# Kernel tuning notes

Hardware: AMD Instinct MI355X
Metric: run time of the kernel (lower is better)

The kernel has to match this reference:

```python
import jax, jax.numpy as jnp
import numpy as np

NEG_SLOPE = 0.2
EPS = 1e-5

N_NODES = 50000
N_GRAPHS = 500
NODES_PER_GRAPH = 100
N_EDGES = 500000
F_IN = 16
F_GRAPH = 4
HID = 64
N_CLASSES = 2


def setup_inputs() -> dict:
    key = jax.random.key(0)
    ks = jax.random.split(key, 32)
    x = jax.random.normal(ks[0], (N_NODES, F_IN), dtype=jnp.float32)
    # intra-graph random edges: dst lives in the same 100-node block as src
    src = jax.random.randint(ks[1], (N_EDGES,), 0, N_NODES)
    dst = (src // NODES_PER_GRAPH) * NODES_PER_GRAPH + jax.random.randint(ks[2], (N_EDGES,), 0, NODES_PER_GRAPH)
    edge_index = jnp.stack([src, dst]).astype(jnp.int64)
    graph_input = jax.random.normal(ks[3], (N_GRAPHS, F_GRAPH), dtype=jnp.float32)
    batch = (jnp.arange(N_NODES) // NODES_PER_GRAPH).astype(jnp.int64)

    def w(k, shape, scale=0.1):
        return (jax.random.normal(k, shape, dtype=jnp.float32) * scale)

    inp = dict(x=x, edge_index=edge_index, graph_input=graph_input, batch=batch)
    # GraphNorm params
    inp['gn_w'] = jnp.ones((F_IN,), jnp.float32)
    inp['gn_b'] = w(ks[4], (F_IN,))
    inp['gn_ms'] = jnp.ones((F_IN,), jnp.float32)
    inp['W1'] = w(ks[5], (F_IN, 4 * HID))
    inp['as1'] = w(ks[6], (4, HID)); inp['ad1'] = w(ks[7], (4, HID))
    inp['b1'] = w(ks[8], (4 * HID,))
    inp['W2'] = w(ks[9], (4 * HID, 4 * HID))
    inp['as2'] = w(ks[10], (4, HID)); inp['ad2'] = w(ks[11], (4, HID))
    inp['b2'] = w(ks[12], (4 * HID,))
    inp['W3'] = w(ks[13], (4 * HID, HID))
    inp['as3'] = w(ks[14], (1, HID)); inp['ad3'] = w(ks[15], (1, HID))
    inp['b3'] = w(ks[16], (HID,))
    # BatchNorm1d (eval mode) over [HID + F_GRAPH]
    D = HID + F_GRAPH
    inp['bn_g'] = 1.0 + w(ks[17], (D,))
    inp['bn_b'] = w(ks[18], (D,))
    inp['bn_m'] = jnp.zeros((D,), jnp.float32)
    inp['bn_v'] = jnp.ones((D,), jnp.float32)
    # Dense head
    inp['Wd1'] = w(ks[19], (D, HID)); inp['bd1'] = w(ks[20], (HID,))
    inp['Wd2'] = w(ks[21], (HID, HID)); inp['bd2'] = w(ks[22], (HID,))
    inp['Wo'] = w(ks[23], (HID, N_CLASSES)); inp['bo'] = w(ks[24], (N_CLASSES,))
    return inp


def _segment_softmax(e, seg, n):
    m = jax.ops.segment_max(e, seg, num_segments=n)
    ex = jnp.exp(e - m[seg])
    s = jax.ops.segment_sum(ex, seg, num_segments=n)
    return ex / s[seg]


def _gat_conv(x, src, dst, W, att_src, att_dst, b):
    N = x.shape[0]
    H, C = att_src.shape
    loop = jnp.arange(N)
    src = jnp.concatenate([src, loop])  # PyG GATConv adds self-loops
    dst = jnp.concatenate([dst, loop])
    h = (x @ W).reshape(N, H, C)
    a_src = (h * att_src).sum(-1)  # [N,H]
    a_dst = (h * att_dst).sum(-1)
    e = jax.nn.leaky_relu(a_src[src] + a_dst[dst], NEG_SLOPE)  # [E,H]
    alpha = _segment_softmax(e, dst, N)
    out = jax.ops.segment_sum(h[src] * alpha[:, :, None], dst, num_segments=N)
    return out.reshape(N, H * C) + b


def _graph_norm(x, batch, n_graphs, w, b, ms):
    cnt = jax.ops.segment_sum(jnp.ones((x.shape[0],), x.dtype), batch, num_segments=n_graphs)[:, None]
    mean = jax.ops.segment_sum(x, batch, num_segments=n_graphs) / cnt
    out = x - mean[batch] * ms
    var = jax.ops.segment_sum(out * out, batch, num_segments=n_graphs) / cnt
    return w * out / jnp.sqrt(var[batch] + EPS) + b


def _global_mean_pool(x, batch, n_graphs):
    cnt = jax.ops.segment_sum(jnp.ones((x.shape[0],), x.dtype), batch, num_segments=n_graphs)[:, None]
    return jax.ops.segment_sum(x, batch, num_segments=n_graphs) / cnt


def reference(x, edge_index, graph_input, batch,
              gn_w, gn_b, gn_ms,
              W1, as1, ad1, b1,
              W2, as2, ad2, b2,
              W3, as3, ad3, b3,
              bn_g, bn_b, bn_m, bn_v,
              Wd1, bd1, Wd2, bd2, Wo, bo):
    src, dst = edge_index[0], edge_index[1]
    G = graph_input.shape[0]
    h = _graph_norm(x, batch, G, gn_w, gn_b, gn_ms)
    # dropout is a no-op in eval
    h = jax.nn.elu(_gat_conv(h, src, dst, W1, as1, ad1, b1))
    h = jax.nn.elu(_gat_conv(h, src, dst, W2, as2, ad2, b2))
    h = _gat_conv(h, src, dst, W3, as3, ad3, b3)
    g = _global_mean_pool(h, batch, G)
    g = jnp.concatenate([g, graph_input], axis=1)
    g = (g - bn_m) / jnp.sqrt(bn_v + EPS) * bn_g + bn_b  # BatchNorm1d eval
    g = jax.nn.selu(g @ Wd1 + bd1)
    g = jax.nn.selu(g @ Wd2 + bd2)
    g = g @ Wo + bo
    return jax.nn.softmax(g, axis=1)
```

## Files before the change

kernel.cpp:

```cpp
#include <hip/hip_runtime.h>
#include <math.h>

#define N_NODES 50000
#define N_ROWS_PAD 50048
#define N_GRAPHS 500
#define NPG 100
#define N_EDGES 500000
#define F_IN 16
#define HID 64
#define EW_CAP 1408

#define SELU_SCALE 1.0507009873554804934193349852946f
#define SELU_ALPHA 1.6732632423543772848170429916717f

typedef __attribute__((ext_vector_type(8))) short short8;
typedef __attribute__((ext_vector_type(8))) unsigned short ushort8;
typedef __attribute__((ext_vector_type(4))) float floatx4;

__device__ __forceinline__ float lrelu(float x){ return x > 0.f ? x : 0.2f * x; }
__device__ __forceinline__ float eluf(float x){ return x > 0.f ? x : expf(x) - 1.f; }
__device__ __forceinline__ float seluf(float x){
    return x > 0.f ? SELU_SCALE * x : SELU_SCALE * (SELU_ALPHA * (expf(x) - 1.f));
}
__device__ __forceinline__ unsigned short f2bf(float x){
    unsigned u = __float_as_uint(x);
    return (unsigned short)((u + 0x7FFFu + ((u >> 16) & 1u)) >> 16);
}
__device__ __forceinline__ float bf2f(unsigned short u){
    return __uint_as_float((unsigned)u << 16);
}
__device__ __forceinline__ float bf2f_lo(unsigned u){
    return __uint_as_float(u << 16);
}
__device__ __forceinline__ float bf2f_hi(unsigned u){
    return __uint_as_float(u & 0xFFFF0000u);
}

__global__ void k_count(const int* __restrict__ dst, int* __restrict__ counts){
    int e = blockIdx.x * 256 + threadIdx.x;
    if (e < N_EDGES) atomicAdd(&counts[dst[e]], 1);
}

__global__ void k_local_scan(const int* __restrict__ counts, int* __restrict__ local_off,
                             int* __restrict__ graph_tot){
    __shared__ int s[128];
    int g = blockIdx.x, t = threadIdx.x;
    int v = (t < NPG) ? counts[g * NPG + t] : 0;
    s[t] = v; __syncthreads();
    for (int o = 1; o < 128; o <<= 1){
        int x = (t >= o) ? s[t - o] : 0;
        __syncthreads();
        s[t] += x;
        __syncthreads();
    }
    if (t < NPG) local_off[g * NPG + t] = s[t] - v;
    if (t == 127) graph_tot[g] = s[127];
}

__global__ void k_graph_scan(const int* __restrict__ graph_tot, int* __restrict__ graph_base){
    __shared__ int s[512];
    int t = threadIdx.x;
    int v = (t < N_GRAPHS) ? graph_tot[t] : 0;
    s[t] = v; __syncthreads();
    for (int o = 1; o < 512; o <<= 1){
        int x = (t >= o) ? s[t - o] : 0;
        __syncthreads();
        s[t] += x;
        __syncthreads();
    }
    if (t < N_GRAPHS) graph_base[t] = s[t] - v;
}

__global__ void k_off(const int* __restrict__ local_off, const int* __restrict__ graph_base,
                      int* __restrict__ node_off, int* __restrict__ write_ptr){
    int n = blockIdx.x * 256 + threadIdx.x;
    if (n < N_NODES){
        int v = local_off[n] + graph_base[n / NPG];
        node_off[n] = v;
        write_ptr[n] = v;
    }
}

__global__ void k_scatter(const int* __restrict__ src, const int* __restrict__ dst,
                          int* __restrict__ write_ptr, int* __restrict__ csr){
    int e = blockIdx.x * 256 + threadIdx.x;
    if (e < N_EDGES){
        int d = dst[e];
        int pos = atomicAdd(&write_ptr[d], 1);
        int b = (d / NPG) * NPG;
        csr[pos] = (src[e] - b) | ((d - b) << 8);
    }
}

__global__ void k_gnorm(const float* __restrict__ x, const float* __restrict__ w,
                        const float* __restrict__ b, const float* __restrict__ ms,
                        float* __restrict__ y){
    __shared__ float sx[NPG * F_IN];
    __shared__ float red[16][16];
    __shared__ float meanS[16], varS[16];
    int g = blockIdx.x, t = threadIdx.x;
    for (int idx = t; idx < NPG * F_IN; idx += 256) sx[idx] = x[g * NPG * F_IN + idx];
    __syncthreads();
    int f = t & 15, grp = t >> 4;
    float p = 0.f;
    for (int i = grp; i < NPG; i += 16) p += sx[i * 16 + f];
    red[grp][f] = p; __syncthreads();
    if (t < 16){
        float s = 0.f;
        for (int i = 0; i < 16; i++) s += red[i][t];
        meanS[t] = s * (1.f / 100.f);
    }
    __syncthreads();
    float mm = meanS[f] * ms[f];
    p = 0.f;
    for (int i = grp; i < NPG; i += 16){ float v = sx[i * 16 + f] - mm; p += v * v; }
    red[grp][f] = p; __syncthreads();
    if (t < 16){
        float s = 0.f;
        for (int i = 0; i < 16; i++) s += red[i][t];
        varS[t] = s * (1.f / 100.f);
    }
    __syncthreads();
    for (int idx = t; idx < NPG * F_IN; idx += 256){
        int ff = idx & 15;
        float v = sx[idx] - meanS[ff] * ms[ff];
        y[g * NPG * F_IN + idx] = w[ff] * v * rsqrtf(varS[ff] + 1e-5f) + b[ff];
    }
}

__global__ void __launch_bounds__(256)
k_gemm_tiled(const float* __restrict__ X, const float* __restrict__ W,
             unsigned short* __restrict__ Ybf, int N){
    __shared__ float As[64][17];
    __shared__ float Bs[16][256];
    int t = threadIdx.x;
    int r0 = blockIdx.x * 64;
    {
        int row = t >> 2, kq = t & 3;
        float4 v = (r0 + row < N) ? *(const float4*)&X[(size_t)(r0 + row) * 16 + kq * 4]
                                  : make_float4(0.f, 0.f, 0.f, 0.f);
        As[row][kq * 4 + 0] = v.x; As[row][kq * 4 + 1] = v.y;
        As[row][kq * 4 + 2] = v.z; As[row][kq * 4 + 3] = v.w;
    }
    for (int i = t; i < 1024; i += 256)
        *(float4*)&Bs[0][i * 4] = *(const float4*)&W[i * 4];
    __syncthreads();

    int c4 = t & 15, rsub = t >> 4;
    float acc[4][16];
    #pragma unroll
    for (int i = 0; i < 4; i++)
        #pragma unroll
        for (int j = 0; j < 16; j++) acc[i][j] = 0.f;

    for (int k = 0; k < 16; k++){
        float a_[4];
        #pragma unroll
        for (int i = 0; i < 4; i++) a_[i] = As[rsub + 16 * i][k];
        float4 b0 = *(const float4*)&Bs[k][c4 * 4];
        float4 b1 = *(const float4*)&Bs[k][64 + c4 * 4];
        float4 b2 = *(const float4*)&Bs[k][128 + c4 * 4];
        float4 b3 = *(const float4*)&Bs[k][192 + c4 * 4];
        float bv[16] = {b0.x, b0.y, b0.z, b0.w, b1.x, b1.y, b1.z, b1.w,
                        b2.x, b2.y, b2.z, b2.w, b3.x, b3.y, b3.z, b3.w};
        #pragma unroll
        for (int i = 0; i < 4; i++)
            #pragma unroll
            for (int j = 0; j < 16; j++) acc[i][j] = fmaf(a_[i], bv[j], acc[i][j]);
    }
    #pragma unroll
    for (int i = 0; i < 4; i++){
        int row = r0 + rsub + 16 * i;
        if (row < N){
            ushort8 ua, ub;
            #pragma unroll
            for (int m = 0; m < 8; m++){
                ua[m] = f2bf(acc[i][(m & 3) * 4 + (m >> 2)]);
                ub[m] = f2bf(acc[i][(m & 3) * 4 + 2 + (m >> 2)]);
            }
            *(ushort8*)&Ybf[(size_t)row * 256 + c4 * 16]     = ua;
            *(ushort8*)&Ybf[(size_t)row * 256 + c4 * 16 + 8] = ub;
        }
    }
}

__global__ void k_pack_w(const float* __restrict__ W, unsigned short* __restrict__ Wp,
                         int K, int OUT){
    int idx = blockIdx.x * 256 + threadIdx.x;
    if (idx >= K * OUT) return;
    int k = idx / OUT, n = idx - k * OUT;
    Wp[(((k >> 3) * OUT) + n) * 8 + (k & 7)] = f2bf(W[idx]);
}

template<int COLB>
__global__ void __launch_bounds__(256)
k_gemm_mfma(const unsigned short* __restrict__ Xb,
            const unsigned short* __restrict__ Wp,
            unsigned short* __restrict__ Ybf, int N, int K, int OUT){
    int b = blockIdx.x;
    if (COLB == 4){
        int xcd = b & 7, idx = b >> 3;
        b = xcd * (int)(gridDim.x >> 3) + idx;
    }
    int cb = b & (COLB - 1);
    int rb = b / COLB;

    int t = threadIdx.x;
    int wave = t >> 6, lane = t & 63;
    int quad = lane >> 4, ln = lane & 15;
    int r0 = rb * 64 + wave * 16;
    int c0 = cb * 64;

    floatx4 acc[4];
    #pragma unroll
    for (int f = 0; f < 4; f++) acc[f] = (floatx4){0.f, 0.f, 0.f, 0.f};

    const unsigned short* aptr = Xb + (size_t)(r0 + ln) * K + quad * 8;
    for (int kt = 0; kt < K; kt += 32){
        short8 a = *(const short8*)(aptr + kt);
        int kc = (kt >> 3) + quad;
        #pragma unroll
        for (int f = 0; f < 4; f++){
            short8 bfr = *(const short8*)(Wp + ((size_t)kc * OUT + c0 + f * 16 + ln) * 8);
            acc[f] = __builtin_amdgcn_mfma_f32_16x16x32_bf16(a, bfr, acc[f], 0, 0, 0);
        }
    }
    int rowb = r0 + quad * 4;
    #pragma unroll
    for (int f = 0; f < 4; f++){
        int col = c0 + f * 16 + ln;
        #pragma unroll
        for (int rg = 0; rg < 4; rg++){
            int row = rowb + rg;
            if (row < N) Ybf[(size_t)row * OUT + col] = f2bf(acc[f][rg]);
        }
    }
}

template<int ILVIN>
__global__ void __launch_bounds__(512)
k_fused4(const unsigned short* __restrict__ hbf, const float* __restrict__ as,
         const float* __restrict__ ad, const float* __restrict__ bias,
         const int* __restrict__ csr, const int* __restrict__ noff,
         const int* __restrict__ cnt, unsigned short* __restrict__ out_bf){
    __shared__ __align__(16) unsigned short hl[NPG * 256];
    __shared__ __align__(16) unsigned int edl[EW_CAP][4];
    __shared__ __align__(16) float asrcl[NPG * 4], adstl[NPG * 4];
    __shared__ __align__(16) float wselfl[NPG * 4], rsuml[NPG * 4];
    __shared__ int offl[NPG], cntl[NPG];

    int g = blockIdx.x, t = threadIdx.x;
    int wave = t >> 6, lane = t & 63;
    int base = g * NPG;

    int ebeg = noff[base];
    int etot = noff[base + NPG - 1] + cnt[base + NPG - 1] - ebeg;
    int eln = etot < EW_CAP ? etot : EW_CAP;

    if (ILVIN){
        const ushort8* hsrc = (const ushort8*)(hbf + (size_t)base * 256);
        for (int i = t; i < NPG * 32; i += 512) ((ushort8*)hl)[i] = hsrc[i];
    } else {
        for (int i = t; i < NPG * 16; i += 512){
            int node = i >> 4, c4 = i & 15;
            const unsigned short* hr = hbf + (size_t)(base + node) * 256 + c4 * 4;
            ushort4 f0 = *(const ushort4*)(hr);
            ushort4 f1 = *(const ushort4*)(hr + 64);
            ushort4 f2 = *(const ushort4*)(hr + 128);
            ushort4 f3 = *(const ushort4*)(hr + 192);
            ushort8 lo, hi;
            lo[0] = f0.x; lo[1] = f1.x; lo[2] = f2.x; lo[3] = f3.x;
            lo[4] = f0.y; lo[5] = f1.y; lo[6] = f2.y; lo[7] = f3.y;
            hi[0] = f0.z; hi[1] = f1.z; hi[2] = f2.z; hi[3] = f3.z;
            hi[4] = f0.w; hi[5] = f1.w; hi[6] = f2.w; hi[7] = f3.w;
            *(ushort8*)&hl[node * 256 + c4 * 16]     = lo;
            *(ushort8*)&hl[node * 256 + c4 * 16 + 8] = hi;
        }
    }
    for (int i = t; i < eln; i += 512) edl[i][2] = (unsigned)csr[ebeg + i];
    if (t < NPG){ offl[t] = noff[base + t]; cntl[t] = cnt[base + t]; }
    __syncthreads();

    {
        int cl = lane & 15, nsub = lane >> 4;
        float av[4][4], dv[4][4];
        #pragma unroll
        for (int hh = 0; hh < 4; hh++){
            float4 a4 = *(const float4*)&as[hh * 64 + cl * 4];
            float4 d4 = *(const float4*)&ad[hh * 64 + cl * 4];
            av[hh][0] = a4.x; av[hh][1] = a4.y; av[hh][2] = a4.z; av[hh][3] = a4.w;
            dv[hh][0] = d4.x; dv[hh][1] = d4.y; dv[hh][2] = d4.z; dv[hh][3] = d4.w;
        }
        for (int g0 = wave * 4; g0 < NPG; g0 += 32){
            int n = g0 + nsub;
            ushort8 lo = *(const ushort8*)&hl[n * 256 + cl * 16];
            ushort8 hi = *(const ushort8*)&hl[n * 256 + cl * 16 + 8];
            float ps[4] = {0.f, 0.f, 0.f, 0.f}, pd[4] = {0.f, 0.f, 0.f, 0.f};
            #pragma unroll
            for (int k = 0; k < 2; k++){
                #pragma unroll
                for (int hh = 0; hh < 4; hh++){
                    float x = bf2f(lo[k * 4 + hh]);
                    ps[hh] = fmaf(x, av[hh][k], ps[hh]);
                    pd[hh] = fmaf(x, dv[hh][k], pd[hh]);
                }
            }
            #pragma unroll
            for (int k = 0; k < 2; k++){
                #pragma unroll
                for (int hh = 0; hh < 4; hh++){
                    float x = bf2f(hi[k * 4 + hh]);
                    ps[hh] = fmaf(x, av[hh][k + 2], ps[hh]);
                    pd[hh] = fmaf(x, dv[hh][k + 2], pd[hh]);
                }
            }
            #pragma unroll
            for (int o = 8; o >= 1; o >>= 1){
                #pragma unroll
                for (int hh = 0; hh < 4; hh++){
                    ps[hh] += __shfl_xor(ps[hh], o);
                    pd[hh] += __shfl_xor(pd[hh], o);
                }
            }
            if (cl == 0){
                *(float4*)&asrcl[n * 4] = make_float4(ps[0], ps[1], ps[2], ps[3]);
                *(float4*)&adstl[n * 4] = make_float4(pd[0], pd[1], pd[2], pd[3]);
            }
        }
    }
    __syncthreads();

    for (int i = t; i < eln; i += 512){
        unsigned sd = edl[i][2];
        int s = sd & 0xFF, d = sd >> 8;
        float4 av = *(const float4*)&asrcl[s * 4];
        float4 dv = *(const float4*)&adstl[d * 4];
        unsigned w0 = f2bf(expf(lrelu(av.x + dv.x)));
        unsigned w1 = f2bf(expf(lrelu(av.y + dv.y)));
        unsigned w2 = f2bf(expf(lrelu(av.z + dv.z)));
        unsigned w3 = f2bf(expf(lrelu(av.w + dv.w)));
        edl[i][0] = w0 | (w1 << 16);
        edl[i][1] = w2 | (w3 << 16);
    }
    __syncthreads();

    if (t < NPG){
        int d = t;
        float4 av = *(const float4*)&asrcl[d * 4];
        float4 dv = *(const float4*)&adstl[d * 4];
        float ws0 = expf(lrelu(av.x + dv.x));
        float ws1 = expf(lrelu(av.y + dv.y));
        float ws2 = expf(lrelu(av.z + dv.z));
        float ws3 = expf(lrelu(av.w + dv.w));
        float s0 = ws0, s1 = ws1, s2 = ws2, s3 = ws3;
        int ebg = offl[d] - ebeg, n = cntl[d];
        for (int j = 0; j < n; j++){
            uint2 v = *(const uint2*)&edl[ebg + j][0];
            s0 += bf2f_lo(v.x); s1 += bf2f_hi(v.x);
            s2 += bf2f_lo(v.y); s3 += bf2f_hi(v.y);
        }
        *(float4*)&wselfl[d * 4] = make_float4(ws0, ws1, ws2, ws3);
        *(float4*)&rsuml[d * 4]  = make_float4(1.f / s0, 1.f / s1, 1.f / s2, 1.f / s3);
    }
    __syncthreads();

    float b0 = bias[lane], b1 = bias[64 + lane], b2 = bias[128 + lane], b3 = bias[192 + lane];
    for (int d = wave; d < NPG; d += 8){
        float4 ws = *(const float4*)&wselfl[d * 4];
        float4 rs = *(const float4*)&rsuml[d * 4];
        ushort4 hv = *(const ushort4*)&hl[d * 256 + lane * 4];
        float a0 = ws.x * bf2f(hv.x);
        float a1 = ws.y * bf2f(hv.y);
        float a2 = ws.z * bf2f(hv.z);
        float a3 = ws.w * bf2f(hv.w);
        int ebg = offl[d] - ebeg, n = cntl[d];
        int j = 0;
        #pragma unroll 1
        for (; j + 4 <= n; j += 4){
            #pragma unroll
            for (int k = 0; k < 4; k++){
                uint4 v = *(const uint4*)&edl[ebg + j + k][0];
                int s = (int)(v.z & 0xFFu);
                ushort4 x = *(const ushort4*)&hl[s * 256 + lane * 4];
                a0 = fmaf(bf2f_lo(v.x), bf2f(x.x), a0);
                a1 = fmaf(bf2f_hi(v.x), bf2f(x.y), a1);
                a2 = fmaf(bf2f_lo(v.y), bf2f(x.z), a2);
                a3 = fmaf(bf2f_hi(v.y), bf2f(x.w), a3);
            }
        }
        for (; j < n; j++){
            uint4 v = *(const uint4*)&edl[ebg + j][0];
            int s = (int)(v.z & 0xFFu);
            ushort4 x = *(const ushort4*)&hl[s * 256 + lane * 4];
            a0 = fmaf(bf2f_lo(v.x), bf2f(x.x), a0);
            a1 = fmaf(bf2f_hi(v.x), bf2f(x.y), a1);
            a2 = fmaf(bf2f_lo(v.y), bf2f(x.z), a2);
            a3 = fmaf(bf2f_hi(v.y), bf2f(x.w), a3);
        }
        size_t ob = (size_t)(base + d) * 256 + lane;
        out_bf[ob]       = f2bf(eluf(a0 * rs.x + b0));
        out_bf[ob + 64]  = f2bf(eluf(a1 * rs.y + b1));
        out_bf[ob + 128] = f2bf(eluf(a2 * rs.z + b2));
        out_bf[ob + 192] = f2bf(eluf(a3 * rs.w + b3));
    }
}

__global__ void __launch_bounds__(256)
k_fused1(const unsigned short* __restrict__ hbf, const float* __restrict__ as,
         const float* __restrict__ ad, const float* __restrict__ bias,
         const int* __restrict__ csr, const int* __restrict__ noff,
         const int* __restrict__ cnt, float* __restrict__ out){
    __shared__ __align__(16) unsigned short hl[NPG * 64];
    __shared__ __align__(16) unsigned int edl[EW_CAP][2];
    __shared__ float asrcl[NPG], adstl[NPG];
    __shared__ float wselfl[NPG], rsuml[NPG];
    __shared__ int offl[NPG], cntl[NPG];

    int g = blockIdx.x, t = threadIdx.x;
    int wave = t >> 6, lane = t & 63;
    int base = g * NPG;

    int ebeg = noff[base];
    int etot = noff[base + NPG - 1] + cnt[base + NPG - 1] - ebeg;
    int eln = etot < EW_CAP ? etot : EW_CAP;

    const ushort8* hsrc = (const ushort8*)(hbf + (size_t)base * 64);
    for (int i = t; i < NPG * 8; i += 256) ((ushort8*)hl)[i] = hsrc[i];
    for (int i = t; i < eln; i += 256) edl[i][1] = (unsigned)csr[ebeg + i];
    if (t < NPG){ offl[t] = noff[base + t]; cntl[t] = cnt[base + t]; }
    __syncthreads();

    {
        int cl = lane & 15, nsub = lane >> 4;
        float4 a4 = *(const float4*)&as[cl * 4];
        float4 d4 = *(const float4*)&ad[cl * 4];
        for (int g0 = wave * 4; g0 < NPG; g0 += 16){
            int n = g0 + nsub;
            ushort4 u = *(const ushort4*)&hl[n * 64 + cl * 4];
            float x0 = bf2f(u.x), x1 = bf2f(u.y), x2 = bf2f(u.z), x3 = bf2f(u.w);
            float ps = x0 * a4.x + x1 * a4.y + x2 * a4.z + x3 * a4.w;
            float pd = x0 * d4.x + x1 * d4.y + x2 * d4.z + x3 * d4.w;
            #pragma unroll
            for (int o = 8; o >= 1; o >>= 1){
                ps += __shfl_xor(ps, o);
                pd += __shfl_xor(pd, o);
            }
            if (cl == 0){ asrcl[n] = ps; adstl[n] = pd; }
        }
    }
    __syncthreads();

    for (int i = t; i < eln; i += 256){
        unsigned sd = edl[i][1];
        int s = sd & 0xFF, d = sd >> 8;
        edl[i][0] = (unsigned)f2bf(expf(lrelu(asrcl[s] + adstl[d])));
    }
    __syncthreads();

    if (t < NPG){
        float wsf = expf(lrelu(asrcl[t] + adstl[t]));
        float sum = wsf;
        int ebg = offl[t] - ebeg, n = cntl[t];
        for (int j = 0; j < n; j++) sum += bf2f((unsigned short)edl[ebg + j][0]);
        wselfl[t] = wsf;
        rsuml[t] = 1.f / sum;
    }
    __syncthreads();

    float bl = bias[lane];
    for (int d = wave; d < NPG; d += 4){
        float acc = wselfl[d] * bf2f(hl[d * 64 + lane]);
        int ebg = offl[d] - ebeg, n = cntl[d];
        for (int j = 0; j < n; j++){
            uint2 v = *(const uint2*)&edl[ebg + j][0];
            acc = fmaf(bf2f_lo(v.x), bf2f(hl[(int)(v.y & 0xFFu) * 64 + lane]), acc);
        }
        out[(size_t)(base + d) * 64 + lane] = acc * rsuml[d] + bl;
    }
}

__global__ void k_head(const float* __restrict__ x3, const float* __restrict__ gin,
                       const float* __restrict__ bn_g, const float* __restrict__ bn_b,
                       const float* __restrict__ bn_m, const float* __restrict__ bn_v,
                       const float* __restrict__ Wd1, const float* __restrict__ bd1,
                       const float* __restrict__ Wd2, const float* __restrict__ bd2,
                       const float* __restrict__ Wo, const float* __restrict__ bo,
                       float* __restrict__ out){
    __shared__ float red[256];
    __shared__ float gv[68];
    __shared__ float g2[64];
    __shared__ float g3[64];
    int g = blockIdx.x, t = threadIdx.x;
    int c = t & 63, grp = t >> 6;
    float p = 0.f;
    for (int i = grp; i < NPG; i += 4) p += x3[(g * NPG + i) * 64 + c];
    red[t] = p; __syncthreads();
    if (t < 64){
        float s = red[t] + red[t + 64] + red[t + 128] + red[t + 192];
        float mean = s * (1.f / 100.f);
        gv[t] = (mean - bn_m[t]) * rsqrtf(bn_v[t] + 1e-5f) * bn_g[t] + bn_b[t];
    } else if (t < 68){
        int j = t - 64;
        float v = gin[g * 4 + j];
        gv[t] = (v - bn_m[t]) * rsqrtf(bn_v[t] + 1e-5f) * bn_g[t] + bn_b[t];
    }
    __syncthreads();
    if (t < 64){
        float s = bd1[t];
        for (int i = 0; i < 68; i++) s += gv[i] * Wd1[i * 64 + t];
        g2[t] = seluf(s);
    }
    __syncthreads();
    if (t < 64){
        float s = bd2[t];
        for (int i = 0; i < 64; i++) s += g2[i] * Wd2[i * 64 + t];
        g3[t] = seluf(s);
    }
    __syncthreads();
    if (t == 0){
        float l0 = bo[0], l1 = bo[1];
        for (int i = 0; i < 64; i++){ l0 += g3[i] * Wo[i * 2]; l1 += g3[i] * Wo[i * 2 + 1]; }
        float mx = fmaxf(l0, l1);
        float e0 = expf(l0 - mx), e1 = expf(l1 - mx);
        float inv = 1.f / (e0 + e1);
        out[g * 2] = e0 * inv;
        out[g * 2 + 1] = e1 * inv;
    }
}

extern "C" void kernel_launch(void* const* d_in, const int* in_sizes, int n_in,
                              void* d_out, int out_size, void* d_ws, size_t ws_size,
                              hipStream_t stream){
    const float* x   = (const float*)d_in[0];
    const int*   ei  = (const int*)d_in[1];
    const float* gin = (const float*)d_in[2];
    const float* gn_w = (const float*)d_in[4];
    const float* gn_b = (const float*)d_in[5];
    const float* gn_ms = (const float*)d_in[6];
    const float* W1 = (const float*)d_in[7];
    const float* as1 = (const float*)d_in[8];
    const float* ad1 = (const float*)d_in[9];
    const float* b1 = (const float*)d_in[10];
    const float* W2 = (const float*)d_in[11];
    const float* as2 = (const float*)d_in[12];
    const float* ad2 = (const float*)d_in[13];
    const float* b2 = (const float*)d_in[14];
    const float* W3 = (const float*)d_in[15];
    const float* as3 = (const float*)d_in[16];
    const float* ad3 = (const float*)d_in[17];
    const float* b3 = (const float*)d_in[18];
    const float* bn_g = (const float*)d_in[19];
    const float* bn_b = (const float*)d_in[20];
    const float* bn_m = (const float*)d_in[21];
    const float* bn_v = (const float*)d_in[22];
    const float* Wd1 = (const float*)d_in[23];
    const float* bd1 = (const float*)d_in[24];
    const float* Wd2 = (const float*)d_in[25];
    const float* bd2 = (const float*)d_in[26];
    const float* Wo = (const float*)d_in[27];
    const float* bo = (const float*)d_in[28];
    float* out = (float*)d_out;

    const int* src = ei;
    const int* dst = ei + N_EDGES;

    char* ws = (char*)d_ws;
    size_t off = 0;
    auto alloc = [&](size_t bytes) -> void* {
        void* p = ws + off;
        off = (off + bytes + 255) & ~(size_t)255;
        return p;
    };
    int* counts     = (int*)alloc((size_t)N_NODES * 4);
    int* local_off  = (int*)alloc((size_t)N_NODES * 4);
    int* node_off   = (int*)alloc((size_t)N_NODES * 4);
    int* write_ptr  = (int*)alloc((size_t)N_NODES * 4);
    int* graph_tot  = (int*)alloc(512 * 4);
    int* graph_base = (int*)alloc(512 * 4);
    int* csr        = (int*)alloc((size_t)N_EDGES * 4);
    float* y        = (float*)alloc((size_t)N_NODES * F_IN * 4);
    unsigned short* wp2 = (unsigned short*)alloc((size_t)256 * 256 * 2);
    unsigned short* wp3 = (unsigned short*)alloc((size_t)256 * 64 * 2);
    unsigned short* xbh = (unsigned short*)alloc((size_t)N_NODES * 256 * 2);
    unsigned short* xb  = (unsigned short*)alloc((size_t)N_ROWS_PAD * 256 * 2);
    unsigned short* x3b = (unsigned short*)alloc((size_t)N_NODES * HID * 2);
    float* bufD     = (float*)alloc((size_t)N_NODES * HID * 4);

    hipMemsetAsync(counts, 0, (size_t)N_NODES * 4, stream);
    k_count<<<(N_EDGES + 255) / 256, 256, 0, stream>>>(dst, counts);
    k_local_scan<<<N_GRAPHS, 128, 0, stream>>>(counts, local_off, graph_tot);
    k_graph_scan<<<1, 512, 0, stream>>>(graph_tot, graph_base);
    k_off<<<(N_NODES + 255) / 256, 256, 0, stream>>>(local_off, graph_base, node_off, write_ptr);
    k_scatter<<<(N_EDGES + 255) / 256, 256, 0, stream>>>(src, dst, write_ptr, csr);

    k_pack_w<<<(256 * 256 + 255) / 256, 256, 0, stream>>>(W2, wp2, 256, 256);
    k_pack_w<<<(256 * 64 + 255) / 256, 256, 0, stream>>>(W3, wp3, 256, 64);

    k_gnorm<<<N_GRAPHS, 256, 0, stream>>>(x, gn_w, gn_b, gn_ms, y);

    k_gemm_tiled<<<(N_NODES + 63) / 64, 256, 0, stream>>>(y, W1, xbh, N_NODES);
    k_fused4<1><<<N_GRAPHS, 512, 0, stream>>>(xbh, as1, ad1, b1, csr, node_off, counts, xb);

    k_gemm_mfma<4><<<(N_ROWS_PAD / 64) * 4, 256, 0, stream>>>(xb, wp2, xbh, N_NODES, 256, 256);
    k_fused4<0><<<N_GRAPHS, 512, 0, stream>>>(xbh, as2, ad2, b2, csr, node_off, counts, xb);

    k_gemm_mfma<1><<<N_ROWS_PAD / 64, 256, 0, stream>>>(xb, wp3, x3b, N_NODES, 256, 64);
    k_fused1<<<N_GRAPHS, 256, 0, stream>>>(x3b, as3, ad3, b3, csr, node_off, counts, bufD);

    k_head<<<N_GRAPHS, 256, 0, stream>>>(bufD, gin, bn_g, bn_b, bn_m, bn_v,
                                         Wd1, bd1, Wd2, bd2, Wo, bo, out);
}
```

Baseline: 357.0 us.

## Fold attention vectors into weights and compute GAT logits inside GEMMs

Precomputes W·a_src and W·a_dst products so per-node attention logits come from the input features: layer 1 in the graph-norm kernel, layers 2 and 3 as an extra MFMA tile inside the GEMM. The aggregation kernels no longer compute logits from the bf16 features and load them from small buffers instead. For layer 1 and layer 3 the feature tile is no longer staged in shared memory; gathers read global memory directly, and k_fused1 moves to 512 threads. Logits now come from bf16-rounded folded weights and inputs rather than the bf16 GEMM outputs, which changes rounding. The direct global gathers rely on cache hits instead of LDS.

```diff
diff --git a/kernel.cpp b/kernel.cpp
--- a/kernel.cpp
+++ b/kernel.cpp
@@ -92,9 +92,57 @@
     }
 }
 
+__global__ void k_prep(const float* __restrict__ W1, const float* __restrict__ as1,
+                       const float* __restrict__ ad1,
+                       const float* __restrict__ W2, const float* __restrict__ as2,
+                       const float* __restrict__ ad2,
+                       const float* __restrict__ W3, const float* __restrict__ as3,
+                       const float* __restrict__ ad3,
+                       unsigned short* __restrict__ Wp2, unsigned short* __restrict__ Wp3,
+                       float* __restrict__ M1f,
+                       unsigned short* __restrict__ Mp2, unsigned short* __restrict__ Mp3){
+    int id = blockIdx.x * 256 + threadIdx.x;
+    if (id < 65536){
+        int k = id >> 8, n = id & 255;
+        Wp2[(((k >> 3) * 256) + n) * 8 + (k & 7)] = f2bf(W2[id]);
+    } else if (id < 81920){
+        int i = id - 65536;
+        int k = i >> 6, n = i & 63;
+        Wp3[(((k >> 3) * 64) + n) * 8 + (k & 7)] = f2bf(W3[i]);
+    } else if (id < 82048){
+        int i = id - 81920;
+        int k = i >> 3, j = i & 7;
+        int h = j & 3;
+        const float* a = (j < 4) ? as1 : ad1;
+        float s = 0.f;
+        for (int c = 0; c < 64; c++) s += W1[k * 256 + h * 64 + c] * a[h * 64 + c];
+        M1f[k * 8 + j] = s;
+    } else if (id < 86144){
+        int i = id - 82048;
+        int k = i >> 4, col = i & 15;
+        float s = 0.f;
+        if (col < 8){
+            int h = col & 3;
+            const float* a = (col < 4) ? as2 : ad2;
+            for (int c = 0; c < 64; c++) s += W2[k * 256 + h * 64 + c] * a[h * 64 + c];
+        }
+        Mp2[((k >> 3) * 16 + col) * 8 + (k & 7)] = f2bf(s);
+    } else if (id < 90240){
+        int i = id - 86144;
+        int k = i >> 4, col = i & 15;
+        float s = 0.f;
+        if (col < 2){
+            const float* a = (col == 0) ? as3 : ad3;
+            for (int c = 0; c < 64; c++) s += W3[k * 64 + c] * a[c];
+        }
+        Mp3[((k >> 3) * 16 + col) * 8 + (k & 7)] = f2bf(s);
+    }
+}
+
 __global__ void k_gnorm(const float* __restrict__ x, const float* __restrict__ w,
                         const float* __restrict__ b, const float* __restrict__ ms,
-                        float* __restrict__ y){
+                        const float* __restrict__ M1f,
+                        float* __restrict__ y, float* __restrict__ lg1){
     __shared__ float sx[NPG * F_IN];
     __shared__ float red[16][16];
     __shared__ float meanS[16], varS[16];
@@ -123,8 +171,17 @@
     __syncthreads();
     for (int idx = t; idx < NPG * F_IN; idx += 256){
         int ff = idx & 15;
-        float v = sx[idx] - meanS[ff] * ms[ff];
-        y[g * NPG * F_IN + idx] = w[ff] * v * rsqrtf(varS[ff] + 1e-5f) + b[ff];
+        float v = w[ff] * (sx[idx] - meanS[ff] * ms[ff]) * rsqrtf(varS[ff] + 1e-5f) + b[ff];
+        sx[idx] = v;
+        y[g * NPG * F_IN + idx] = v;
+    }
+    __syncthreads();
+    for (int i = t; i < NPG * 8; i += 256){
+        int n = i >> 3, j = i & 7;
+        float s = 0.f;
+        #pragma unroll
+        for (int ff = 0; ff < 16; ff++) s += sx[n * 16 + ff] * M1f[ff * 8 + j];
+        lg1[(size_t)(g * NPG + n) * 8 + j] = s;
     }
 }
 
@@ -184,19 +241,13 @@
     }
 }
 
-__global__ void k_pack_w(const float* __restrict__ W, unsigned short* __restrict__ Wp,
-                         int K, int OUT){
-    int idx = blockIdx.x * 256 + threadIdx.x;
-    if (idx >= K * OUT) return;
-    int k = idx / OUT, n = idx - k * OUT;
-    Wp[(((k >> 3) * OUT) + n) * 8 + (k & 7)] = f2bf(W[idx]);
-}
-
-template<int COLB>
+template<int COLB, int LG>
 __global__ void __launch_bounds__(256)
 k_gemm_mfma(const unsigned short* __restrict__ Xb,
             const unsigned short* __restrict__ Wp,
-            unsigned short* __restrict__ Ybf, int N, int K, int OUT){
+            const unsigned short* __restrict__ Mp,
+            unsigned short* __restrict__ Ybf, float* __restrict__ lg,
+            int N, int K, int OUT){
     int b = blockIdx.x;
     if (COLB == 4){
         int xcd = b & 7, idx = b >> 3;
@@ -214,6 +265,7 @@
     floatx4 acc[4];
     #pragma unroll
     for (int f = 0; f < 4; f++) acc[f] = (floatx4){0.f, 0.f, 0.f, 0.f};
+    floatx4 accL = (floatx4){0.f, 0.f, 0.f, 0.f};
 
     const unsigned short* aptr = Xb + (size_t)(r0 + ln) * K + quad * 8;
     for (int kt = 0; kt < K; kt += 32){
@@ -224,6 +276,12 @@
             short8 bfr = *(const short8*)(Wp + ((size_t)kc * OUT + c0 + f * 16 + ln) * 8);
             acc[f] = __builtin_amdgcn_mfma_f32_16x16x32_bf16(a, bfr, acc[f], 0, 0, 0);
         }
+        if (LG > 0){
+            if (cb == 0){
+                short8 m = *(const short8*)(Mp + ((size_t)kc * 16 + ln) * 8);
+                accL = __builtin_amdgcn_mfma_f32_16x16x32_bf16(a, m, accL, 0, 0, 0);
+            }
+        }
     }
     int rowb = r0 + quad * 4;
     #pragma unroll
@@ -235,15 +293,24 @@
             if (row < N) Ybf[(size_t)row * OUT + col] = f2bf(acc[f][rg]);
         }
     }
+    if (LG > 0){
+        if (cb == 0 && ln < LG){
+            #pragma unroll
+            for (int rg = 0; rg < 4; rg++){
+                int row = rowb + rg;
+                if (row < N) lg[(size_t)row * LG + ln] = accL[rg];
+            }
+        }
+    }
 }
 
 template<int ILVIN>
 __global__ void __launch_bounds__(512)
-k_fused4(const unsigned short* __restrict__ hbf, const float* __restrict__ as,
-         const float* __restrict__ ad, const float* __restrict__ bias,
+k_fused4(const unsigned short* __restrict__ hbf, const float* __restrict__ lg,
+         const float* __restrict__ bias,
          const int* __restrict__ csr, const int* __restrict__ noff,
          const int* __restrict__ cnt, unsigned short* __restrict__ out_bf){
-    __shared__ __align__(16) unsigned short hl[NPG * 256];
+    __shared__ __align__(16) unsigned short hl[ILVIN ? 16 : NPG * 256];
     __shared__ __align__(16) unsigned int edl[EW_CAP][4];
     __shared__ __align__(16) float asrcl[NPG * 4], adstl[NPG * 4];
     __shared__ __align__(16) float wselfl[NPG * 4], rsuml[NPG * 4];
@@ -257,10 +324,7 @@
     int etot = noff[base + NPG - 1] + cnt[base + NPG - 1] - ebeg;
     int eln = etot < EW_CAP ? etot : EW_CAP;
 
-    if (ILVIN){
-        const ushort8* hsrc = (const ushort8*)(hbf + (size_t)base * 256);
-        for (int i = t; i < NPG * 32; i += 512) ((ushort8*)hl)[i] = hsrc[i];
-    } else {
+    if (!ILVIN){
         for (int i = t; i < NPG * 16; i += 512){
             int node = i >> 4, c4 = i & 15;
             const unsigned short* hr = hbf + (size_t)(base + node) * 256 + c4 * 4;
@@ -278,55 +342,12 @@
         }
     }
     for (int i = t; i < eln; i += 512) edl[i][2] = (unsigned)csr[ebeg + i];
-    if (t < NPG){ offl[t] = noff[base + t]; cntl[t] = cnt[base + t]; }
-    __syncthreads();
-
-    {
-        int cl = lane & 15, nsub = lane >> 4;
-        float av[4][4], dv[4][4];
-        #pragma unroll
-        for (int hh = 0; hh < 4; hh++){
-            float4 a4 = *(const float4*)&as[hh * 64 + cl * 4];
-            float4 d4 = *(const float4*)&ad[hh * 64 + cl * 4];
-            av[hh][0] = a4.x; av[hh][1] = a4.y; av[hh][2] = a4.z; av[hh][3] = a4.w;
-            dv[hh][0] = d4.x; dv[hh][1] = d4.y; dv[hh][2] = d4.z; dv[hh][3] = d4.w;
-        }
-        for (int g0 = wave * 4; g0 < NPG; g0 += 32){
-            int n = g0 + nsub;
-            ushort8 lo = *(const ushort8*)&hl[n * 256 + cl * 16];
-            ushort8 hi = *(const ushort8*)&hl[n * 256 + cl * 16 + 8];
-            float ps[4] = {0.f, 0.f, 0.f, 0.f}, pd[4] = {0.f, 0.f, 0.f, 0.f};
-            #pragma unroll
-            for (int k = 0; k < 2; k++){
-                #pragma unroll
-                for (int hh = 0; hh < 4; hh++){
-                    float x = bf2f(lo[k * 4 + hh]);
-                    ps[hh] = fmaf(x, av[hh][k], ps[hh]);
-                    pd[hh] = fmaf(x, dv[hh][k], pd[hh]);
-                }
-            }
-            #pragma unroll
-            for (int k = 0; k < 2; k++){
-                #pragma unroll
-                for (int hh = 0; hh < 4; hh++){
-                    float x = bf2f(hi[k * 4 + hh]);
-                    ps[hh] = fmaf(x, av[hh][k + 2], ps[hh]);
-                    pd[hh] = fmaf(x, dv[hh][k + 2], pd[hh]);
-                }
-            }
-            #pragma unroll
-            for (int o = 8; o >= 1; o >>= 1){
-                #pragma unroll
-                for (int hh = 0; hh < 4; hh++){
-                    ps[hh] += __shfl_xor(ps[hh], o);
-                    pd[hh] += __shfl_xor(pd[hh], o);
-                }
-            }
-            if (cl == 0){
-                *(float4*)&asrcl[n * 4] = make_float4(ps[0], ps[1], ps[2], ps[3]);
-                *(float4*)&adstl[n * 4] = make_float4(pd[0], pd[1], pd[2], pd[3]);
-            }
-        }
+    if (t < NPG){
+        offl[t] = noff[base + t];
+        cntl[t] = cnt[base + t];
+        const float* lp = lg + (size_t)(base + t) * 8;
+        *(float4*)&asrcl[t * 4] = *(const float4*)lp;
+        *(float4*)&adstl[t * 4] = *(const float4*)(lp + 4);
     }
     __syncthreads();
 
@@ -368,7 +389,8 @@
     for (int d = wave; d < NPG; d += 8){
         float4 ws = *(const float4*)&wselfl[d * 4];
         float4 rs = *(const float4*)&rsuml[d * 4];
-        ushort4 hv = *(const ushort4*)&hl[d * 256 + lane * 4];
+        ushort4 hv = ILVIN ? *(const ushort4*)&hbf[(size_t)(base + d) * 256 + lane * 4]
+                           : *(const ushort4*)&hl[d * 256 + lane * 4];
         float a0 = ws.x * bf2f(hv.x);
         float a1 = ws.y * bf2f(hv.y);
         float a2 = ws.z * bf2f(hv.z);
@@ -381,7 +403,8 @@
             for (int k = 0; k < 4; k++){
                 uint4 v = *(const uint4*)&edl[ebg + j + k][0];
                 int s = (int)(v.z & 0xFFu);
-                ushort4 x = *(const ushort4*)&hl[s * 256 + lane * 4];
+                ushort4 x = ILVIN ? *(const ushort4*)&hbf[(size_t)(base + s) * 256 + lane * 4]
+                                  : *(const ushort4*)&hl[s * 256 + lane * 4];
                 a0 = fmaf(bf2f_lo(v.x), bf2f(x.x), a0);
                 a1 = fmaf(bf2f_hi(v.x), bf2f(x.y), a1);
                 a2 = fmaf(bf2f_lo(v.y), bf2f(x.z), a2);
@@ -391,7 +414,8 @@
         for (; j < n; j++){
             uint4 v = *(const uint4*)&edl[ebg + j][0];
             int s = (int)(v.z & 0xFFu);
-            ushort4 x = *(const ushort4*)&hl[s * 256 + lane * 4];
+            ushort4 x = ILVIN ? *(const ushort4*)&hbf[(size_t)(base + s) * 256 + lane * 4]
+                              : *(const ushort4*)&hl[s * 256 + lane * 4];
             a0 = fmaf(bf2f_lo(v.x), bf2f(x.x), a0);
             a1 = fmaf(bf2f_hi(v.x), bf2f(x.y), a1);
             a2 = fmaf(bf2f_lo(v.y), bf2f(x.z), a2);
@@ -405,12 +429,11 @@
     }
 }
 
-__global__ void __launch_bounds__(256)
-k_fused1(const unsigned short* __restrict__ hbf, const float* __restrict__ as,
-         const float* __restrict__ ad, const float* __restrict__ bias,
+__global__ void __launch_bounds__(512)
+k_fused1(const unsigned short* __restrict__ hbf, const float* __restrict__ lg3,
+         const float* __restrict__ bias,
          const int* __restrict__ csr, const int* __restrict__ noff,
          const int* __restrict__ cnt, float* __restrict__ out){
-    __shared__ __align__(16) unsigned short hl[NPG * 64];
     __shared__ __align__(16) unsigned int edl[EW_CAP][2];
     __shared__ float asrcl[NPG], adstl[NPG];
     __shared__ float wselfl[NPG], rsuml[NPG];
@@ -424,33 +447,16 @@
     int etot = noff[base + NPG - 1] + cnt[base + NPG - 1] - ebeg;
     int eln = etot < EW_CAP ? etot : EW_CAP;
 
-    const ushort8* hsrc = (const ushort8*)(hbf + (size_t)base * 64);
-    for (int i = t; i < NPG * 8; i += 256) ((ushort8*)hl)[i] = hsrc[i];
-    for (int i = t; i < eln; i += 256) edl[i][1] = (unsigned)csr[ebeg + i];
-    if (t < NPG){ offl[t] = noff[base + t]; cntl[t] = cnt[base + t]; }
-    __syncthreads();
-
-    {
-        int cl = lane & 15, nsub = lane >> 4;
-        float4 a4 = *(const float4*)&as[cl * 4];
-        float4 d4 = *(const float4*)&ad[cl * 4];
-        for (int g0 = wave * 4; g0 < NPG; g0 += 16){
-            int n = g0 + nsub;
-            ushort4 u = *(const ushort4*)&hl[n * 64 + cl * 4];
-            float x0 = bf2f(u.x), x1 = bf2f(u.y), x2 = bf2f(u.z), x3 = bf2f(u.w);
-            float ps = x0 * a4.x + x1 * a4.y + x2 * a4.z + x3 * a4.w;
-            float pd = x0 * d4.x + x1 * d4.y + x2 * d4.z + x3 * d4.w;
-            #pragma unroll
-            for (int o = 8; o >= 1; o >>= 1){
-                ps += __shfl_xor(ps, o);
-                pd += __shfl_xor(pd, o);
-            }
-            if (cl == 0){ asrcl[n] = ps; adstl[n] = pd; }
-        }
-    }
-    __syncthreads();
-
-    for (int i = t; i < eln; i += 256){
+    for (int i = t; i < eln; i += 512) edl[i][1] = (unsigned)csr[ebeg + i];
+    if (t < NPG){
+        offl[t] = noff[base + t];
+        cntl[t] = cnt[base + t];
+        asrcl[t] = lg3[(size_t)(base + t) * 2];
+        adstl[t] = lg3[(size_t)(base + t) * 2 + 1];
+    }
+    __syncthreads();
+
+    for (int i = t; i < eln; i += 512){
         unsigned sd = edl[i][1];
         int s = sd & 0xFF, d = sd >> 8;
         edl[i][0] = (unsigned)f2bf(expf(lrelu(asrcl[s] + adstl[d])));
@@ -468,12 +474,13 @@
     __syncthreads();
 
     float bl = bias[lane];
-    for (int d = wave; d < NPG; d += 4){
-        float acc = wselfl[d] * bf2f(hl[d * 64 + lane]);
+    for (int d = wave; d < NPG; d += 8){
+        float acc = wselfl[d] * bf2f(hbf[(size_t)(base + d) * 64 + lane]);
         int ebg = offl[d] - ebeg, n = cntl[d];
         for (int j = 0; j < n; j++){
             uint2 v = *(const uint2*)&edl[ebg + j][0];
-            acc = fmaf(bf2f_lo(v.x), bf2f(hl[(int)(v.y & 0xFFu) * 64 + lane]), acc);
+            acc = fmaf(bf2f_lo(v.x),
+                       bf2f(hbf[(size_t)(base + (int)(v.y & 0xFFu)) * 64 + lane]), acc);
         }
         out[(size_t)(base + d) * 64 + lane] = acc * rsuml[d] + bl;
     }
@@ -581,6 +588,12 @@
     float* y        = (float*)alloc((size_t)N_NODES * F_IN * 4);
     unsigned short* wp2 = (unsigned short*)alloc((size_t)256 * 256 * 2);
     unsigned short* wp3 = (unsigned short*)alloc((size_t)256 * 64 * 2);
+    float* M1f      = (float*)alloc((size_t)16 * 8 * 4);
+    unsigned short* Mp2 = (unsigned short*)alloc((size_t)32 * 16 * 8 * 2);
+    unsigned short* Mp3 = (unsigned short*)alloc((size_t)32 * 16 * 8 * 2);
+    float* lg1      = (float*)alloc((size_t)N_NODES * 8 * 4);
+    float* lg2      = (float*)alloc((size_t)N_ROWS_PAD * 8 * 4);
+    float* lg3      = (float*)alloc((size_t)N_ROWS_PAD * 2 * 4);
     unsigned short* xbh = (unsigned short*)alloc((size_t)N_NODES * 256 * 2);
     unsigned short* xb  = (unsigned short*)alloc((size_t)N_ROWS_PAD * 256 * 2);
     unsigned short* x3b = (unsigned short*)alloc((size_t)N_NODES * HID * 2);
@@ -593,19 +606,21 @@
     k_off<<<(N_NODES + 255) / 256, 256, 0, stream>>>(local_off, graph_base, node_off, write_ptr);
     k_scatter<<<(N_EDGES + 255) / 256, 256, 0, stream>>>(src, dst, write_ptr, csr);
 
-    k_pack_w<<<(256 * 256 + 255) / 256, 256, 0, stream>>>(W2, wp2, 256, 256);
-    k_pack_w<<<(256 * 64 + 255) / 256, 256, 0, stream>>>(W3, wp3, 256, 64);
-
-    k_gnorm<<<N_GRAPHS, 256, 0, stream>>>(x, gn_w, gn_b, gn_ms, y);
+    k_prep<<<(90240 + 255) / 256, 256, 0, stream>>>(W1, as1, ad1, W2, as2, ad2,
+                                                    W3, as3, ad3, wp2, wp3, M1f, Mp2, Mp3);
+
+    k_gnorm<<<N_GRAPHS, 256, 0, stream>>>(x, gn_w, gn_b, gn_ms, M1f, y, lg1);
 
     k_gemm_tiled<<<(N_NODES + 63) / 64, 256, 0, stream>>>(y, W1, xbh, N_NODES);
-    k_fused4<1><<<N_GRAPHS, 512, 0, stream>>>(xbh, as1, ad1, b1, csr, node_off, counts, xb);
-
-    k_gemm_mfma<4><<<(N_ROWS_PAD / 64) * 4, 256, 0, stream>>>(xb, wp2, xbh, N_NODES, 256, 256);
-    k_fused4<0><<<N_GRAPHS, 512, 0, stream>>>(xbh, as2, ad2, b2, csr, node_off, counts, xb);
-
-    k_gemm_mfma<1><<<N_ROWS_PAD / 64, 256, 0, stream>>>(xb, wp3, x3b, N_NODES, 256, 64);
-    k_fused1<<<N_GRAPHS, 256, 0, stream>>>(x3b, as3, ad3, b3, csr, node_off, counts, bufD);
+    k_fused4<1><<<N_GRAPHS, 512, 0, stream>>>(xbh, lg1, b1, csr, node_off, counts, xb);
+
+    k_gemm_mfma<4, 8><<<(N_ROWS_PAD / 64) * 4, 256, 0, stream>>>(xb, wp2, Mp2, xbh, lg2,
+                                                                 N_NODES, 256, 256);
+    k_fused4<0><<<N_GRAPHS, 512, 0, stream>>>(xbh, lg2, b2, csr, node_off, counts, xb);
+
+    k_gemm_mfma<1, 2><<<N_ROWS_PAD / 64, 256, 0, stream>>>(xb, wp3, Mp3, x3b, lg3,
+                                                           N_NODES, 256, 64);
+    k_fused1<<<N_GRAPHS, 512, 0, stream>>>(x3b, lg3, b3, csr, node_off, counts, bufD);
 
     k_head<<<N_GRAPHS, 256, 0, stream>>>(bufD, gin, bn_g, bn_b, bn_m, bn_v,
                                          Wd1, bd1, Wd2, bd2, Wo, bo, out);
```

After: 349.8 us. -2.0%, faster.
